# Kernel optimization log

Measured on AMD Instinct MI355X. Metric: run time of the kernel, lower is better.

## Reference

```python
import jax, jax.numpy as jnp
import numpy as np

B, Q, S, H, D = 4, 1024, 2048, 32, 128  # batch, new tokens, cache capacity, heads, head_dim
SCALE = 0.08838834764831845  # 1/sqrt(128)


def setup_inputs() -> dict:
    key = jax.random.key(0)
    ks = jax.random.split(key, 7)
    query_states = jax.random.normal(ks[0], (B, Q, H, D), jnp.float32)
    key_states = jax.random.normal(ks[1], (B, Q, H, D), jnp.float32)
    value_states = jax.random.normal(ks[2], (B, Q, H, D), jnp.float32)
    k_cache = jax.random.normal(ks[3], (B, S, H, D), jnp.float32)
    v_cache = jax.random.normal(ks[4], (B, S, H, D), jnp.float32)
    q_lens = jax.random.randint(ks[5], (B,), 1, Q + 1).astype(jnp.int32)      # ragged new lengths
    cache_lens = jax.random.randint(ks[6], (B,), 0, Q + 1).astype(jnp.int32)  # prior context lengths
    return dict(query_states=query_states, key_states=key_states, value_states=value_states,
                k_cache=k_cache, v_cache=v_cache, q_lens=q_lens, cache_lens=cache_lens)


def _update_cache(cache, new, cache_lens, q_lens):
    # Per-sequence append: write new[b, :q_len[b]] into cache[b, cache_len[b]:cache_len[b]+q_len[b]]
    def upd(c, n, clen, qlen):
        j = jnp.arange(Q)
        idx = jnp.clip(clen + j, 0, S - 1)               # [Q]
        valid = j < qlen                                  # [Q]
        vals = jnp.where(valid[:, None, None], n, c[idx])  # keep old value where padded
        return c.at[idx].set(vals)
    return jax.vmap(upd)(cache, new, cache_lens, q_lens)


def reference(query_states, key_states, value_states, k_cache, v_cache, q_lens, cache_lens):
    kc = _update_cache(k_cache, key_states, cache_lens, q_lens)   # [B,S,H,D]
    vc = _update_cache(v_cache, value_states, cache_lens, q_lens)

    scores = jnp.einsum('bqhd,bkhd->bhqk', query_states, kc) * SCALE  # [B,H,Q,S]

    qi = jnp.arange(Q)
    kj = jnp.arange(S)
    # query i may attend to cache pos j iff j < cache_len + min(i+1, q_len)  (causal + segment bound)
    limit = cache_lens[:, None] + jnp.minimum(qi[None, :] + 1, q_lens[:, None])  # [B,Q]
    mask = kj[None, None, :] < limit[:, :, None]                                  # [B,Q,S]
    scores = jnp.where(mask[:, None, :, :], scores, -jnp.inf)
    probs = jax.nn.softmax(scores, axis=-1)

    out = jnp.einsum('bhqk,bkhd->bqhd', probs, vc)  # [B,Q,H,D]
    q_valid = (qi[None, :] < q_lens[:, None])[:, :, None, None]
    return jnp.where(q_valid, out, jnp.zeros((), out.dtype))
```

## Files before the change

### kernel.cpp

```cpp
#include <hip/hip_runtime.h>


#define BB 4
#define QQ 1024
#define SS 2048
#define HH 32
#define DD 128
#define KT 32
#define NTILES 64
#define TILE_ELEMS 4096
#define NPERQ 256

typedef __attribute__((ext_vector_type(8))) short short8;
typedef __attribute__((ext_vector_type(4))) float f32x4;
typedef __attribute__((ext_vector_type(16))) float f32x16;
typedef __attribute__((ext_vector_type(4))) unsigned int u32x4;
typedef __attribute__((ext_vector_type(8))) unsigned short u16x8;

__device__ __forceinline__ unsigned short f2bf(float f) {
    unsigned int u = __builtin_bit_cast(unsigned int, f);
    u += 0x7FFFu + ((u >> 16) & 1u);
    return (unsigned short)(u >> 16);
}
__device__ __forceinline__ unsigned int cvtpk(float lo, float hi) {
    unsigned int r;
    asm("v_cvt_pk_bf16_f32 %0, %1, %2" : "=v"(r) : "v"(lo), "v"(hi));
    return r;
}
__device__ __forceinline__ void glds16(const unsigned short* g, unsigned short* l) {
    __builtin_amdgcn_global_load_lds(
        (const __attribute__((address_space(1))) unsigned int*)g,
        (__attribute__((address_space(3))) unsigned int*)l, 16, 0, 0);
}

__global__ __launch_bounds__(256)
void prep(const float* __restrict__ ks, const float* __restrict__ vs,
          const float* __restrict__ kc_, const float* __restrict__ vc,
          const int* __restrict__ qlens, const int* __restrict__ clens,
          unsigned short* __restrict__ Kws, unsigned short* __restrict__ Vws)
{
    const int tile = blockIdx.x, h = blockIdx.y, b = blockIdx.z;
    const int qlen = qlens[b], clen = clens[b];
    if (tile * KT >= clen + qlen) return;
    const int tid = threadIdx.x;
    unsigned short* kout = Kws + (((size_t)b * HH + h) * NTILES + tile) * TILE_ELEMS;
    unsigned short* vout = Vws + (((size_t)b * HH + h) * NTILES + tile) * TILE_ELEMS;

    #pragma unroll
    for (int h2 = 0; h2 < 2; ++h2) {
        const int idx8 = h2 * 2048 + tid * 8;
        const int c = idx8 >> 9, l = (idx8 >> 3) & 63;
        int key = tile * KT + (l & 31);
        const float* src;
        if (key < clen) {
            src = kc_ + (((size_t)b * SS + key) * HH + h) * DD;
        } else {
            int i2 = key - clen; if (i2 > QQ - 1) i2 = QQ - 1;
            src = ks + (((size_t)b * QQ + i2) * HH + h) * DD;
        }
        const int d0 = c * 16 + ((l >> 5) << 3);
        f32x4 a0 = *(const f32x4*)&src[d0];
        f32x4 a1 = *(const f32x4*)&src[d0 + 4];
        u16x8 w;
        w[0] = f2bf(a0[0]); w[1] = f2bf(a0[1]); w[2] = f2bf(a0[2]); w[3] = f2bf(a0[3]);
        w[4] = f2bf(a1[0]); w[5] = f2bf(a1[1]); w[6] = f2bf(a1[2]); w[7] = f2bf(a1[3]);
        *(u16x8*)&kout[idx8] = w;
    }
    #pragma unroll
    for (int h2 = 0; h2 < 2; ++h2) {
        const int idx8 = h2 * 2048 + tid * 8;
        const int a = idx8 >> 9, l = (idx8 >> 3) & 63;
        const int dchunk = a >> 1, kcc = a & 1;
        const int d = dchunk * 32 + (l & 31);
        const int kb = tile * KT + kcc * 16 + ((l >> 5) << 3);
        u16x8 w;
        #pragma unroll
        for (int e = 0; e < 8; ++e) {
            int key = kb + e;
            const float* src;
            if (key < clen) {
                src = vc + (((size_t)b * SS + key) * HH + h) * DD;
            } else {
                int i2 = key - clen; if (i2 > QQ - 1) i2 = QQ - 1;
                src = vs + (((size_t)b * QQ + i2) * HH + h) * DD;
            }
            w[e] = f2bf(src[d]);
        }
        *(u16x8*)&vout[idx8] = w;
    }
}

#define TSTEP(T, SC, SN, BC, BN)                                                \
{                                                                               \
    const int pbase = (T) * KT;                                                 \
    const int t2c = ((T) + 2 < nt) ? (T) + 2 : (nt - 1);                        \
    const unsigned short* k2p = Kb + (size_t)t2c * TILE_ELEMS;                  \
    _Pragma("unroll")                                                           \
    for (int j = 0; j < 4; ++j)                                                 \
        glds16(&k2p[sbase + j * 512], &KVl[BC][lbase + j * 512]);               \
    if (pbase + KT > lim_min) {                                                 \
        _Pragma("unroll")                                                       \
        for (int r = 0; r < 16; ++r) {                                          \
            const int kk = pbase + (r & 3) + ((r >> 2) << 3) + hi * 4;          \
            if (kk >= lim_l) SC[r] = -3e38f;                                    \
        }                                                                       \
    }                                                                           \
    float pm = fmaxf(fmaxf(fmaxf(fmaxf(SC[0], SC[1]), fmaxf(SC[2], SC[3])),     \
                           fmaxf(fmaxf(SC[4], SC[5]), fmaxf(SC[6], SC[7]))),    \
                     fmaxf(fmaxf(fmaxf(SC[8], SC[9]), fmaxf(SC[10], SC[11])),   \
                           fmaxf(fmaxf(SC[12], SC[13]), fmaxf(SC[14], SC[15])))); \
    if (__any(pm > m_ + 8.0f)) {                                                \
        pm = fmaxf(pm, __shfl_xor(pm, 32));                                     \
        const float mn = fmaxf(m_, pm);                                         \
        const float alpha = __builtin_amdgcn_exp2f(m_ - mn);                    \
        m_ = mn;                                                                \
        l_ *= alpha;                                                            \
        _Pragma("unroll")                                                       \
        for (int r = 0; r < 16; ++r) {                                          \
            o0[r] *= alpha; o1[r] *= alpha; o2[r] *= alpha; o3[r] *= alpha;     \
        }                                                                       \
    }                                                                           \
    float p[16];                                                                \
    _Pragma("unroll")                                                           \
    for (int r = 0; r < 16; ++r) p[r] = __builtin_amdgcn_exp2f(SC[r] - m_);     \
    l_ += (((p[0]+p[1])+(p[2]+p[3])) + ((p[4]+p[5])+(p[6]+p[7])))               \
        + (((p[8]+p[9])+(p[10]+p[11])) + ((p[12]+p[13])+(p[14]+p[15])));        \
    const unsigned int w0 = cvtpk(p[0],  p[1]);                                 \
    const unsigned int w1 = cvtpk(p[2],  p[3]);                                 \
    const unsigned int w2 = cvtpk(p[4],  p[5]);                                 \
    const unsigned int w3 = cvtpk(p[6],  p[7]);                                 \
    const unsigned int w4 = cvtpk(p[8],  p[9]);                                 \
    const unsigned int w5 = cvtpk(p[10], p[11]);                                \
    const unsigned int w6 = cvtpk(p[12], p[13]);                                \
    const unsigned int w7 = cvtpk(p[14], p[15]);                                \
    const unsigned int x0 = (unsigned int)__shfl_xor((int)w0, 32);              \
    const unsigned int x1 = (unsigned int)__shfl_xor((int)w1, 32);              \
    const unsigned int x2 = (unsigned int)__shfl_xor((int)w2, 32);              \
    const unsigned int x3 = (unsigned int)__shfl_xor((int)w3, 32);              \
    const unsigned int x4 = (unsigned int)__shfl_xor((int)w4, 32);              \
    const unsigned int x5 = (unsigned int)__shfl_xor((int)w5, 32);              \
    const unsigned int x6 = (unsigned int)__shfl_xor((int)w6, 32);              \
    const unsigned int x7 = (unsigned int)__shfl_xor((int)w7, 32);              \
    u32x4 pb0w, pb1w;                                                           \
    pb0w[0] = hiL ? x2 : w0;  pb0w[1] = hiL ? x3 : w1;                          \
    pb0w[2] = hiL ? w2 : x0;  pb0w[3] = hiL ? w3 : x1;                          \
    pb1w[0] = hiL ? x6 : w4;  pb1w[1] = hiL ? x7 : w5;                          \
    pb1w[2] = hiL ? w6 : x4;  pb1w[3] = hiL ? w7 : x5;                          \
    const short8 pb0 = __builtin_bit_cast(short8, pb0w);                        \
    const short8 pb1 = __builtin_bit_cast(short8, pb1w);                        \
    asm volatile("s_waitcnt vmcnt(4)" ::: "memory");                            \
    __builtin_amdgcn_s_barrier();                                               \
    __builtin_amdgcn_sched_barrier(0);                                          \
    SN = (f32x16){0.f};                                                         \
    __builtin_amdgcn_s_setprio(1);                                              \
    _Pragma("unroll")                                                           \
    for (int c = 0; c < 8; ++c) {                                               \
        short8 kf = *(const short8*)&KVl[BN][c * 512 + lane * 8];               \
        SN = __builtin_amdgcn_mfma_f32_32x32x16_bf16(kf, qf[c], SN, 0, 0, 0);   \
    }                                                                           \
    {                                                                           \
        short8 va = *(const short8*)&KVl[BC][4096 + 0 * 512 + lane * 8];        \
        short8 vb = *(const short8*)&KVl[BC][4096 + 1 * 512 + lane * 8];        \
        o0 = __builtin_amdgcn_mfma_f32_32x32x16_bf16(va, pb0, o0, 0, 0, 0);     \
        o0 = __builtin_amdgcn_mfma_f32_32x32x16_bf16(vb, pb1, o0, 0, 0, 0);     \
    }                                                                           \
    {                                                                           \
        short8 va = *(const short8*)&KVl[BC][4096 + 2 * 512 + lane * 8];        \
        short8 vb = *(const short8*)&KVl[BC][4096 + 3 * 512 + lane * 8];        \
        o1 = __builtin_amdgcn_mfma_f32_32x32x16_bf16(va, pb0, o1, 0, 0, 0);     \
        o1 = __builtin_amdgcn_mfma_f32_32x32x16_bf16(vb, pb1, o1, 0, 0, 0);     \
    }                                                                           \
    {                                                                           \
        short8 va = *(const short8*)&KVl[BC][4096 + 4 * 512 + lane * 8];        \
        short8 vb = *(const short8*)&KVl[BC][4096 + 5 * 512 + lane * 8];        \
        o2 = __builtin_amdgcn_mfma_f32_32x32x16_bf16(va, pb0, o2, 0, 0, 0);     \
        o2 = __builtin_amdgcn_mfma_f32_32x32x16_bf16(vb, pb1, o2, 0, 0, 0);     \
    }                                                                           \
    {                                                                           \
        short8 va = *(const short8*)&KVl[BC][4096 + 6 * 512 + lane * 8];        \
        short8 vb = *(const short8*)&KVl[BC][4096 + 7 * 512 + lane * 8];        \
        o3 = __builtin_amdgcn_mfma_f32_32x32x16_bf16(va, pb0, o3, 0, 0, 0);     \
        o3 = __builtin_amdgcn_mfma_f32_32x32x16_bf16(vb, pb1, o3, 0, 0, 0);     \
    }                                                                           \
    __builtin_amdgcn_s_setprio(0);                                              \
    asm volatile("s_waitcnt lgkmcnt(0)" ::: "memory");                          \
    __builtin_amdgcn_s_barrier();                                               \
    __builtin_amdgcn_sched_barrier(0);                                          \
    const unsigned short* v2p = Vb + (size_t)t2c * TILE_ELEMS;                  \
    _Pragma("unroll")                                                           \
    for (int j = 0; j < 4; ++j)                                                 \
        glds16(&v2p[sbase + j * 512], &KVl[BC][4096 + lbase + j * 512]);        \
}

__global__ __launch_bounds__(128, 2)
void segattn_persist(const float* __restrict__ qs, const int* __restrict__ qlens,
                     const int* __restrict__ clens,
                     const unsigned short* __restrict__ Kws,
                     const unsigned short* __restrict__ Vws,
                     float* __restrict__ out, int* __restrict__ counter)
{
    __shared__ int s_item;
    alignas(16) __shared__ unsigned short KVl[2][8192];

    const int tid = threadIdx.x, w = tid >> 6, lane = tid & 63;
    const int q31 = lane & 31, hi = lane >> 5;
    const bool hiL = (hi != 0);
    const float psc = 0.08838834764831845f * 1.4426950408889634f;
    const int sbase = w * 2048 + lane * 8;
    const int lbase = w * 2048;
    const int cres = blockIdx.x & 7;
    int* myctr = counter + cres;

    for (;;) {
        if (tid == 0) s_item = atomicAdd(myctr, 1);
        __syncthreads();
        const int pop = s_item;
        __syncthreads();
        if (pop >= NPERQ) break;

        const int bhi = pop >> 4, qtord = pop & 15;
        const int qt = 15 - qtord;
        const int b = bhi & 3, h = cres + 8 * (bhi >> 2);
        const int qlen = qlens[b], clen = clens[b];
        const int q0 = qt * 64;

        if (q0 >= qlen) {
            f32x4 z = {0.f, 0.f, 0.f, 0.f};
            #pragma unroll
            for (int i2 = 0; i2 < 16; ++i2) {
                int f = tid + i2 * 128;
                int r = f >> 5, d4 = f & 31;
                *(f32x4*)&out[(((size_t)b * QQ + q0 + r) * HH + h) * DD + d4 * 4] = z;
            }
            continue;
        }

        const int q = q0 + w * 32 + q31;
        const float* qp = qs + (((size_t)b * QQ + q) * HH + h) * DD;
        short8 qf[8];
        #pragma unroll
        for (int c = 0; c < 8; ++c) {
            const int d0 = c * 16 + hi * 8;
            f32x4 a0 = *(const f32x4*)&qp[d0];
            f32x4 a1 = *(const f32x4*)&qp[d0 + 4];
            short8 t;
            t[0] = (short)f2bf(a0[0] * psc); t[1] = (short)f2bf(a0[1] * psc);
            t[2] = (short)f2bf(a0[2] * psc); t[3] = (short)f2bf(a0[3] * psc);
            t[4] = (short)f2bf(a1[0] * psc); t[5] = (short)f2bf(a1[1] * psc);
            t[6] = (short)f2bf(a1[2] * psc); t[7] = (short)f2bf(a1[3] * psc);
            qf[c] = t;
        }

        const int lim_l = (q < qlen) ? (clen + q + 1) : 0;
        const int wq0 = q0 + w * 32;
        const int lim_min = (wq0 + 31 < qlen) ? (clen + wq0 + 1) : 0;

        float m_ = -3e38f, l_ = 0.f;
        f32x16 o0 = {0}, o1 = {0}, o2 = {0}, o3 = {0};

        const int kmax = clen + min(q0 + 64, qlen);
        const int nt = (kmax + KT - 1) / KT;
        const unsigned short* Kb = Kws + ((size_t)(b * HH + h)) * NTILES * TILE_ELEMS;
        const unsigned short* Vb = Vws + ((size_t)(b * HH + h)) * NTILES * TILE_ELEMS;

        #pragma unroll
        for (int j = 0; j < 4; ++j) {
            glds16(&Kb[sbase + j * 512], &KVl[0][lbase + j * 512]);
            glds16(&Vb[sbase + j * 512], &KVl[0][4096 + lbase + j * 512]);
        }
        asm volatile("s_waitcnt vmcnt(0)" ::: "memory");
        __builtin_amdgcn_s_barrier();
        __builtin_amdgcn_sched_barrier(0);
        {
            const int t1x = (nt > 1) ? 1 : 0;
            const unsigned short* k1p = Kb + (size_t)t1x * TILE_ELEMS;
            const unsigned short* v1p = Vb + (size_t)t1x * TILE_ELEMS;
            #pragma unroll
            for (int j = 0; j < 4; ++j) {
                glds16(&k1p[sbase + j * 512], &KVl[1][lbase + j * 512]);
                glds16(&v1p[sbase + j * 512], &KVl[1][4096 + lbase + j * 512]);
            }
        }
        f32x16 sA = {0}, sB;
        __builtin_amdgcn_s_setprio(1);
        #pragma unroll
        for (int c = 0; c < 8; ++c) {
            short8 kf = *(const short8*)&KVl[0][c * 512 + lane * 8];
            sA = __builtin_amdgcn_mfma_f32_32x32x16_bf16(kf, qf[c], sA, 0, 0, 0);
        }
        __builtin_amdgcn_s_setprio(0);
        asm volatile("s_waitcnt lgkmcnt(0)" ::: "memory");
        __builtin_amdgcn_s_barrier();
        __builtin_amdgcn_sched_barrier(0);

        int t = 0;
        for (; t + 2 <= nt; t += 2) {
            TSTEP(t,     sA, sB, 0, 1);
            TSTEP(t + 1, sB, sA, 1, 0);
        }
        if (t < nt) {
            TSTEP(t, sA, sB, 0, 1);
        }
        asm volatile("s_waitcnt vmcnt(0)" ::: "memory");

        float lt = l_ + __shfl_xor(l_, 32);
        const bool val = (q < qlen);
        const float inv = val ? (1.0f / lt) : 0.f;
        float* op = out + (((size_t)b * QQ + q) * HH + h) * DD;
        #pragma unroll
        for (int rr = 0; rr < 4; ++rr) {
            f32x4 wv;
            const int d0 = rr * 8 + hi * 4;
            wv[0] = o0[rr*4+0]*inv; wv[1] = o0[rr*4+1]*inv;
            wv[2] = o0[rr*4+2]*inv; wv[3] = o0[rr*4+3]*inv;
            *(f32x4*)&op[d0] = wv;
            wv[0] = o1[rr*4+0]*inv; wv[1] = o1[rr*4+1]*inv;
            wv[2] = o1[rr*4+2]*inv; wv[3] = o1[rr*4+3]*inv;
            *(f32x4*)&op[32 + d0] = wv;
            wv[0] = o2[rr*4+0]*inv; wv[1] = o2[rr*4+1]*inv;
            wv[2] = o2[rr*4+2]*inv; wv[3] = o2[rr*4+3]*inv;
            *(f32x4*)&op[64 + d0] = wv;
            wv[0] = o3[rr*4+0]*inv; wv[1] = o3[rr*4+1]*inv;
            wv[2] = o3[rr*4+2]*inv; wv[3] = o3[rr*4+3]*inv;
            *(f32x4*)&op[96 + d0] = wv;
        }
    }
}

__global__ __launch_bounds__(256)
void segattn(const float* __restrict__ qs, const float* __restrict__ ks,
             const float* __restrict__ vs, const float* __restrict__ kc,
             const float* __restrict__ vc, const int* __restrict__ qlens,
             const int* __restrict__ clens, float* __restrict__ out)
{
    const int qt = blockIdx.x, h = blockIdx.y, b = blockIdx.z;
    const int tid = threadIdx.x, wave = tid >> 6, lane = tid & 63;
    const int g = lane >> 4, lc = lane & 15;
    const int qlen = qlens[b], clen = clens[b];
    const int q0 = qt * 64;
    if (q0 >= qlen) {
        f32x4 z = {0.f, 0.f, 0.f, 0.f};
        #pragma unroll
        for (int i2 = 0; i2 < 8; ++i2) {
            int f = tid + i2 * 256;
            int r = f >> 5, d4 = f & 31;
            *(f32x4*)&out[(((size_t)b * QQ + q0 + r) * HH + h) * DD + d4 * 4] = z;
        }
        return;
    }
    alignas(16) __shared__ unsigned short Kl[KT * DD];
    alignas(16) __shared__ unsigned short Vl[DD * 40];
    alignas(16) __shared__ unsigned short Pl[4][16][40];
    const float psc = 0.08838834764831845f * 1.4426950408889634f;
    const int qrow = q0 + wave * 16 + lc;
    const float* qp = qs + (((size_t)b * QQ + qrow) * HH + h) * DD;
    short8 qf[4];
    #pragma unroll
    for (int c = 0; c < 4; ++c) {
        f32x4 a0 = *(const f32x4*)&qp[c * 32 + g * 8];
        f32x4 a1 = *(const f32x4*)&qp[c * 32 + g * 8 + 4];
        short8 t;
        t[0] = (short)f2bf(a0[0] * psc); t[1] = (short)f2bf(a0[1] * psc);
        t[2] = (short)f2bf(a0[2] * psc); t[3] = (short)f2bf(a0[3] * psc);
        t[4] = (short)f2bf(a1[0] * psc); t[5] = (short)f2bf(a1[1] * psc);
        t[6] = (short)f2bf(a1[2] * psc); t[7] = (short)f2bf(a1[3] * psc);
        qf[c] = t;
    }
    f32x4 o[8];
    #pragma unroll
    for (int n = 0; n < 8; ++n) o[n] = (f32x4){0.f, 0.f, 0.f, 0.f};
    float m_[4] = {-3e38f, -3e38f, -3e38f, -3e38f};
    float l_[4] = {0.f, 0.f, 0.f, 0.f};
    int lim[4];
    #pragma unroll
    for (int qq = 0; qq < 4; ++qq) {
        int i = q0 + wave * 16 + g * 4 + qq;
        lim[qq] = (i < qlen) ? (clen + i + 1) : 0;
    }
    const int kmax = clen + min(q0 + 64, qlen);
    const int nt = (kmax + KT - 1) / KT;
    for (int t = 0; t < nt; ++t) {
        const int pbase = t * KT;
        __syncthreads();
        #pragma unroll
        for (int it = 0; it < 4; ++it) {
            int f = tid + it * 256;
            int key = f >> 5, d4 = f & 31;
            int p = pbase + key;
            const float *srck, *srcv;
            if (p < clen) {
                size_t off = (((size_t)b * SS + p) * HH + h) * DD + d4 * 4;
                srck = kc + off; srcv = vc + off;
            } else {
                int idx = p - clen; if (idx > QQ - 1) idx = QQ - 1;
                size_t off = (((size_t)b * QQ + idx) * HH + h) * DD + d4 * 4;
                srck = ks + off; srcv = vs + off;
            }
            f32x4 kv = *(const f32x4*)srck;
            f32x4 vv = *(const f32x4*)srcv;
            int ei = (key * DD + d4 * 4) ^ ((key & 7) << 3);
            typedef __attribute__((ext_vector_type(4))) unsigned short u16x4;
            u16x4 kb4 = {f2bf(kv[0]), f2bf(kv[1]), f2bf(kv[2]), f2bf(kv[3])};
            *(u16x4*)&Kl[ei] = kb4;
            int d0 = d4 * 4;
            Vl[(d0 + 0) * 40 + key] = f2bf(vv[0]);
            Vl[(d0 + 1) * 40 + key] = f2bf(vv[1]);
            Vl[(d0 + 2) * 40 + key] = f2bf(vv[2]);
            Vl[(d0 + 3) * 40 + key] = f2bf(vv[3]);
        }
        __syncthreads();
        f32x4 sc0 = {0.f, 0.f, 0.f, 0.f}, sc1 = {0.f, 0.f, 0.f, 0.f};
        #pragma unroll
        for (int c = 0; c < 4; ++c) {
            int i0 = (lc * DD + c * 32 + g * 8) ^ ((lc & 7) << 3);
            int i1 = ((16 + lc) * DD + c * 32 + g * 8) ^ (((16 + lc) & 7) << 3);
            short8 k0 = *(const short8*)&Kl[i0];
            short8 k1 = *(const short8*)&Kl[i1];
            sc0 = __builtin_amdgcn_mfma_f32_16x16x32_bf16(qf[c], k0, sc0, 0, 0, 0);
            sc1 = __builtin_amdgcn_mfma_f32_16x16x32_bf16(qf[c], k1, sc1, 0, 0, 0);
        }
        float pr0[4], pr1[4];
        #pragma unroll
        for (int qq = 0; qq < 4; ++qq) {
            float s0 = sc0[qq], s1 = sc1[qq];
            if (pbase + lc >= lim[qq])      s0 = -3e38f;
            if (pbase + 16 + lc >= lim[qq]) s1 = -3e38f;
            float pm = fmaxf(s0, s1);
            #pragma unroll
            for (int d2 = 1; d2 < 16; d2 <<= 1) pm = fmaxf(pm, __shfl_xor(pm, d2));
            float mn = fmaxf(m_[qq], pm);
            float alpha = exp2f(m_[qq] - mn);
            float p0 = exp2f(s0 - mn), p1 = exp2f(s1 - mn);
            float rs = p0 + p1;
            #pragma unroll
            for (int d2 = 1; d2 < 16; d2 <<= 1) rs += __shfl_xor(rs, d2);
            l_[qq] = l_[qq] * alpha + rs;
            m_[qq] = mn;
            pr0[qq] = p0; pr1[qq] = p1;
            #pragma unroll
            for (int n = 0; n < 8; ++n) o[n][qq] *= alpha;
        }
        #pragma unroll
        for (int qq = 0; qq < 4; ++qq) {
            Pl[wave][g * 4 + qq][lc]      = f2bf(pr0[qq]);
            Pl[wave][g * 4 + qq][16 + lc] = f2bf(pr1[qq]);
        }
        short8 pf = *(const short8*)&Pl[wave][lc][g * 8];
        #pragma unroll
        for (int n = 0; n < 8; ++n) {
            short8 vf = *(const short8*)&Vl[(n * 16 + lc) * 40 + g * 8];
            o[n] = __builtin_amdgcn_mfma_f32_16x16x32_bf16(pf, vf, o[n], 0, 0, 0);
        }
    }
    #pragma unroll
    for (int qq = 0; qq < 4; ++qq) {
        int i = q0 + wave * 16 + g * 4 + qq;
        bool val = (i < qlen);
        float inv = val ? (1.0f / l_[qq]) : 0.f;
        size_t ob = (((size_t)b * QQ + i) * HH + h) * DD + lc;
        #pragma unroll
        for (int n = 0; n < 8; ++n)
            out[ob + (size_t)n * 16] = val ? o[n][qq] * inv : 0.f;
    }
}

extern "C" void kernel_launch(void* const* d_in, const int* in_sizes, int n_in,
                              void* d_out, int out_size, void* d_ws, size_t ws_size,
                              hipStream_t stream) {
    const float* qs = (const float*)d_in[0];
    const float* ks = (const float*)d_in[1];
    const float* vs = (const float*)d_in[2];
    const float* kc = (const float*)d_in[3];
    const float* vc = (const float*)d_in[4];
    const int* ql = (const int*)d_in[5];
    const int* cl = (const int*)d_in[6];
    float* o = (float*)d_out;

    const size_t kv_elems = (size_t)BB * HH * NTILES * TILE_ELEMS;
    const size_t kv_bytes = kv_elems * 2 * sizeof(unsigned short);
    const size_t need = kv_bytes + 128;

    if (ws_size >= need) {
        unsigned short* Kws = (unsigned short*)d_ws;
        unsigned short* Vws = Kws + kv_elems;
        int* counter = (int*)((char*)d_ws + kv_bytes);
        hipMemsetAsync(counter, 0, 128, stream);
        dim3 pgrid(NTILES, HH, BB), pblk(256, 1, 1);
        hipLaunchKernelGGL(prep, pgrid, pblk, 0, stream, ks, vs, kc, vc, ql, cl, Kws, Vws);
        dim3 grid(1024, 1, 1), blk(128, 1, 1);
        hipLaunchKernelGGL(segattn_persist, grid, blk, 0, stream, qs, ql, cl, Kws, Vws, o, counter);
    } else {
        dim3 grid(QQ / 64, HH, BB), blk(256, 1, 1);
        hipLaunchKernelGGL(segattn, grid, blk, 0, stream, qs, ks, vs, kc, vc, ql, cl, o);
    }
}
```

Before: 159.5 us.

## Load V tiles directly into registers, halve LDS, raise occupancy

V tiles are no longer staged through double-buffered LDS. Each wave now reads its V fragments for the current tile straight from global memory into registers at the start of each step, and the LDS buffer shrinks to K only. With half the shared memory, the launch bound is raised from 2 to 3 blocks per CU. The trade-off is that global-load latency for V is exposed within each step rather than prefetched two tiles ahead, and both waves fetch the same V data redundantly. The reuse of the existing vmcnt(4) wait with the new load mix also needs care.

```diff
diff --git a/kernel.cpp b/kernel.cpp
--- a/kernel.cpp
+++ b/kernel.cpp
@@ -93,11 +93,20 @@
 #define TSTEP(T, SC, SN, BC, BN)                                                \
 {                                                                               \
     const int pbase = (T) * KT;                                                 \
+    const unsigned short* vtp = Vb + (size_t)(T) * TILE_ELEMS;                  \
+    short8 vf0 = *(const short8*)&vtp[0 * 512 + lane * 8];                      \
+    short8 vf1 = *(const short8*)&vtp[1 * 512 + lane * 8];                      \
+    short8 vf2 = *(const short8*)&vtp[2 * 512 + lane * 8];                      \
+    short8 vf3 = *(const short8*)&vtp[3 * 512 + lane * 8];                      \
+    short8 vf4 = *(const short8*)&vtp[4 * 512 + lane * 8];                      \
+    short8 vf5 = *(const short8*)&vtp[5 * 512 + lane * 8];                      \
+    short8 vf6 = *(const short8*)&vtp[6 * 512 + lane * 8];                      \
+    short8 vf7 = *(const short8*)&vtp[7 * 512 + lane * 8];                      \
     const int t2c = ((T) + 2 < nt) ? (T) + 2 : (nt - 1);                        \
     const unsigned short* k2p = Kb + (size_t)t2c * TILE_ELEMS;                  \
     _Pragma("unroll")                                                           \
     for (int j = 0; j < 4; ++j)                                                 \
-        glds16(&k2p[sbase + j * 512], &KVl[BC][lbase + j * 512]);               \
+        glds16(&k2p[sbase + j * 512], &Kl[BC][lbase + j * 512]);                \
     if (pbase + KT > lim_min) {                                                 \
         _Pragma("unroll")                                                       \
         for (int r = 0; r < 16; ++r) {                                          \
@@ -155,44 +164,24 @@
     __builtin_amdgcn_s_setprio(1);                                              \
     _Pragma("unroll")                                                           \
     for (int c = 0; c < 8; ++c) {                                               \
-        short8 kf = *(const short8*)&KVl[BN][c * 512 + lane * 8];               \
+        short8 kf = *(const short8*)&Kl[BN][c * 512 + lane * 8];                \
         SN = __builtin_amdgcn_mfma_f32_32x32x16_bf16(kf, qf[c], SN, 0, 0, 0);   \
     }                                                                           \
-    {                                                                           \
-        short8 va = *(const short8*)&KVl[BC][4096 + 0 * 512 + lane * 8];        \
-        short8 vb = *(const short8*)&KVl[BC][4096 + 1 * 512 + lane * 8];        \
-        o0 = __builtin_amdgcn_mfma_f32_32x32x16_bf16(va, pb0, o0, 0, 0, 0);     \
-        o0 = __builtin_amdgcn_mfma_f32_32x32x16_bf16(vb, pb1, o0, 0, 0, 0);     \
-    }                                                                           \
-    {                                                                           \
-        short8 va = *(const short8*)&KVl[BC][4096 + 2 * 512 + lane * 8];        \
-        short8 vb = *(const short8*)&KVl[BC][4096 + 3 * 512 + lane * 8];        \
-        o1 = __builtin_amdgcn_mfma_f32_32x32x16_bf16(va, pb0, o1, 0, 0, 0);     \
-        o1 = __builtin_amdgcn_mfma_f32_32x32x16_bf16(vb, pb1, o1, 0, 0, 0);     \
-    }                                                                           \
-    {                                                                           \
-        short8 va = *(const short8*)&KVl[BC][4096 + 4 * 512 + lane * 8];        \
-        short8 vb = *(const short8*)&KVl[BC][4096 + 5 * 512 + lane * 8];        \
-        o2 = __builtin_amdgcn_mfma_f32_32x32x16_bf16(va, pb0, o2, 0, 0, 0);     \
-        o2 = __builtin_amdgcn_mfma_f32_32x32x16_bf16(vb, pb1, o2, 0, 0, 0);     \
-    }                                                                           \
-    {                                                                           \
-        short8 va = *(const short8*)&KVl[BC][4096 + 6 * 512 + lane * 8];        \
-        short8 vb = *(const short8*)&KVl[BC][4096 + 7 * 512 + lane * 8];        \
-        o3 = __builtin_amdgcn_mfma_f32_32x32x16_bf16(va, pb0, o3, 0, 0, 0);     \
-        o3 = __builtin_amdgcn_mfma_f32_32x32x16_bf16(vb, pb1, o3, 0, 0, 0);     \
-    }                                                                           \
+    o0 = __builtin_amdgcn_mfma_f32_32x32x16_bf16(vf0, pb0, o0, 0, 0, 0);        \
+    o0 = __builtin_amdgcn_mfma_f32_32x32x16_bf16(vf1, pb1, o0, 0, 0, 0);        \
+    o1 = __builtin_amdgcn_mfma_f32_32x32x16_bf16(vf2, pb0, o1, 0, 0, 0);        \
+    o1 = __builtin_amdgcn_mfma_f32_32x32x16_bf16(vf3, pb1, o1, 0, 0, 0);        \
+    o2 = __builtin_amdgcn_mfma_f32_32x32x16_bf16(vf4, pb0, o2, 0, 0, 0);        \
+    o2 = __builtin_amdgcn_mfma_f32_32x32x16_bf16(vf5, pb1, o2, 0, 0, 0);        \
+    o3 = __builtin_amdgcn_mfma_f32_32x32x16_bf16(vf6, pb0, o3, 0, 0, 0);        \
+    o3 = __builtin_amdgcn_mfma_f32_32x32x16_bf16(vf7, pb1, o3, 0, 0, 0);        \
     __builtin_amdgcn_s_setprio(0);                                              \
     asm volatile("s_waitcnt lgkmcnt(0)" ::: "memory");                          \
     __builtin_amdgcn_s_barrier();                                               \
     __builtin_amdgcn_sched_barrier(0);                                          \
-    const unsigned short* v2p = Vb + (size_t)t2c * TILE_ELEMS;                  \
-    _Pragma("unroll")                                                           \
-    for (int j = 0; j < 4; ++j)                                                 \
-        glds16(&v2p[sbase + j * 512], &KVl[BC][4096 + lbase + j * 512]);        \
-}
-
-__global__ __launch_bounds__(128, 2)
+}
+
+__global__ __launch_bounds__(128, 3)
 void segattn_persist(const float* __restrict__ qs, const int* __restrict__ qlens,
                      const int* __restrict__ clens,
                      const unsigned short* __restrict__ Kws,
@@ -200,7 +189,7 @@
                      float* __restrict__ out, int* __restrict__ counter)
 {
     __shared__ int s_item;
-    alignas(16) __shared__ unsigned short KVl[2][8192];
+    alignas(16) __shared__ unsigned short Kl[2][4096];
 
     const int tid = threadIdx.x, w = tid >> 6, lane = tid & 63;
     const int q31 = lane & 31, hi = lane >> 5;
@@ -264,28 +253,23 @@
         const unsigned short* Vb = Vws + ((size_t)(b * HH + h)) * NTILES * TILE_ELEMS;
 
         #pragma unroll
-        for (int j = 0; j < 4; ++j) {
-            glds16(&Kb[sbase + j * 512], &KVl[0][lbase + j * 512]);
-            glds16(&Vb[sbase + j * 512], &KVl[0][4096 + lbase + j * 512]);
-        }
+        for (int j = 0; j < 4; ++j)
+            glds16(&Kb[sbase + j * 512], &Kl[0][lbase + j * 512]);
         asm volatile("s_waitcnt vmcnt(0)" ::: "memory");
         __builtin_amdgcn_s_barrier();
         __builtin_amdgcn_sched_barrier(0);
         {
             const int t1x = (nt > 1) ? 1 : 0;
             const unsigned short* k1p = Kb + (size_t)t1x * TILE_ELEMS;
-            const unsigned short* v1p = Vb + (size_t)t1x * TILE_ELEMS;
             #pragma unroll
-            for (int j = 0; j < 4; ++j) {
-                glds16(&k1p[sbase + j * 512], &KVl[1][lbase + j * 512]);
-                glds16(&v1p[sbase + j * 512], &KVl[1][4096 + lbase + j * 512]);
-            }
+            for (int j = 0; j < 4; ++j)
+                glds16(&k1p[sbase + j * 512], &Kl[1][lbase + j * 512]);
         }
         f32x16 sA = {0}, sB;
         __builtin_amdgcn_s_setprio(1);
         #pragma unroll
         for (int c = 0; c < 8; ++c) {
-            short8 kf = *(const short8*)&KVl[0][c * 512 + lane * 8];
+            short8 kf = *(const short8*)&Kl[0][c * 512 + lane * 8];
             sA = __builtin_amdgcn_mfma_f32_32x32x16_bf16(kf, qf[c], sA, 0, 0, 0);
         }
         __builtin_amdgcn_s_setprio(0);
```

Result: slower. 312.5 us (+96.0%).
